# Performance work log

Hardware: AMD Instinct MI355X
Metric: run time of the kernel (lower is better)

The kernel has to match this reference:

```python
import jax, jax.numpy as jnp
import numpy as np


def setup_inputs() -> dict:
    key = jax.random.key(0)
    k1, k2 = jax.random.split(key)
    query_features = jax.random.normal(k1, (8, 2048, 256), dtype=jnp.float32)   # (B, S, D)
    support_weights = jax.random.normal(k2, (20, 256), dtype=jnp.float32)       # (N, D)
    return {"query_features": query_features, "support_weights": support_weights}


def reference(query_features, support_weights):
    # Original: transpose query to (B, D, S), repeat channels n_cls times,
    # grouped conv1d with groups = n_cls*D, group_size=1, kernel_size=1, padding=0.
    # That is exactly a per-(class, channel) scale of the query features.
    B, S, D = query_features.shape
    N = support_weights.shape[0]
    q = jnp.transpose(query_features, (0, 2, 1))            # (B, D, S)
    # out[b, n, c, s] = q[b, c, s] * w[n, c]
    out = q[:, None, :, :] * support_weights[None, :, :, None]  # (B, N, D, S)
    return out.reshape(B * N, D, S)                          # (B*N, D, S)
```

## Files before the change

### kernel.cpp

```cpp
#include <hip/hip_runtime.h>


namespace {
constexpr int kB = 8;
constexpr int kS = 2048;
constexpr int kD = 256;
constexpr int kN = 20;
constexpr int TS = 512;
constexpr int TC = 16;
constexpr int PTS = TS + 4;
}

__global__ __launch_bounds__(256)
void frw_kernel(const float* __restrict__ q, const float* __restrict__ w,
                float* __restrict__ out) {
  const int s0 = blockIdx.x * TS;
  const int c0 = blockIdx.y * TC;
  const int b  = blockIdx.z;
  const int t  = threadIdx.x;

  __shared__ float tile[TC][PTS];
  __shared__ float ws[kN][TC];

  for (int i = t; i < kN * TC; i += 256) {
    const int n  = i / TC;
    const int cc = i % TC;
    ws[n][cc] = w[n * kD + c0 + cc];
  }

  {
    const int lane4 = t & 3;
    const int srow  = t >> 2;
    const int cvec  = lane4 * 4;
#pragma unroll
    for (int k = 0; k < 8; ++k) {
      const int ss = srow + k * 64;
      const float4 v = *reinterpret_cast<const float4*>(
          &q[((size_t)b * kS + (size_t)(s0 + ss)) * kD + (c0 + cvec)]);
      tile[cvec + 0][ss] = v.x;
      tile[cvec + 1][ss] = v.y;
      tile[cvec + 2][ss] = v.z;
      tile[cvec + 3][ss] = v.w;
    }
  }
  __syncthreads();

  const int half = t >> 7;
  const int soff = (t & 127) * 4;
  for (int n = 0; n < kN; ++n) {
    const size_t base_bn = ((size_t)(b * kN + n)) * kD;
#pragma unroll
    for (int rg = 0; rg < TC / 2; ++rg) {
      const int r = rg * 2 + half;
      const float sc = ws[n][r];
      const float4 v = *reinterpret_cast<const float4*>(&tile[r][soff]);
      float4 o;
      o.x = v.x * sc;
      o.y = v.y * sc;
      o.z = v.z * sc;
      o.w = v.w * sc;
      *reinterpret_cast<float4*>(
          &out[(base_bn + (size_t)(c0 + r)) * kS + (size_t)(s0 + soff)]) = o;
    }
  }
}

extern "C" void kernel_launch(void* const* d_in, const int* in_sizes, int n_in,
                              void* d_out, int out_size, void* d_ws, size_t ws_size,
                              hipStream_t stream) {
  const float* q = (const float*)d_in[0];
  const float* w = (const float*)d_in[1];
  float* out = (float*)d_out;

  dim3 grid(kS / TS, kD / TC, kB);
  frw_kernel<<<grid, 256, 0, stream>>>(q, w, out);
}
```

Before: 341.1 us.

## Give each wavefront a full channel row held in registers, with nontemporal stores

The shared-memory transpose tile is replaced by a per-wavefront mapping: each wave owns one channel across the whole sequence. It loads that channel's query values with strided scalar loads into 32 registers and keeps all 20 weights in registers. Output rows are then written as vectorized nontemporal stores so the large write stream does not pollute cache. The change removes LDS traffic and the barrier, but the query reads become uncoalesced strided loads, and the grid shrinks to 512 blocks.

```diff
diff --git a/kernel.cpp b/kernel.cpp
--- a/kernel.cpp
+++ b/kernel.cpp
@@ -6,61 +6,45 @@
 constexpr int kS = 2048;
 constexpr int kD = 256;
 constexpr int kN = 20;
-constexpr int TS = 512;
-constexpr int TC = 16;
-constexpr int PTS = TS + 4;
+
+typedef float v4f __attribute__((ext_vector_type(4)));
 }
 
 __global__ __launch_bounds__(256)
 void frw_kernel(const float* __restrict__ q, const float* __restrict__ w,
                 float* __restrict__ out) {
-  const int s0 = blockIdx.x * TS;
-  const int c0 = blockIdx.y * TC;
-  const int b  = blockIdx.z;
-  const int t  = threadIdx.x;
+  const int lane = threadIdx.x & 63;
+  const int wv   = threadIdx.x >> 6;
+  const int c    = blockIdx.x * 4 + wv;
+  const int b    = blockIdx.y;
 
-  __shared__ float tile[TC][PTS];
-  __shared__ float ws[kN][TC];
+  float wreg[kN];
+#pragma unroll
+  for (int n = 0; n < kN; ++n) wreg[n] = w[n * kD + c];
 
-  for (int i = t; i < kN * TC; i += 256) {
-    const int n  = i / TC;
-    const int cc = i % TC;
-    ws[n][cc] = w[n * kD + c0 + cc];
+  float qv[8][4];
+  const float* qb = q + (size_t)b * kS * kD + c;
+#pragma unroll
+  for (int k = 0; k < 8; ++k) {
+#pragma unroll
+    for (int j = 0; j < 4; ++j) {
+      qv[k][j] = qb[(size_t)(k * 256 + 4 * lane + j) * kD];
+    }
   }
 
-  {
-    const int lane4 = t & 3;
-    const int srow  = t >> 2;
-    const int cvec  = lane4 * 4;
+  float* ob = out + ((size_t)(b * kN) * kD + (size_t)c) * kS + 4 * lane;
+#pragma unroll
+  for (int n = 0; n < kN; ++n) {
+    const float sc = wreg[n];
+    float* orow = ob + (size_t)n * kD * kS;
 #pragma unroll
     for (int k = 0; k < 8; ++k) {
-      const int ss = srow + k * 64;
-      const float4 v = *reinterpret_cast<const float4*>(
-          &q[((size_t)b * kS + (size_t)(s0 + ss)) * kD + (c0 + cvec)]);
-      tile[cvec + 0][ss] = v.x;
-      tile[cvec + 1][ss] = v.y;
-      tile[cvec + 2][ss] = v.z;
-      tile[cvec + 3][ss] = v.w;
-    }
-  }
-  __syncthreads();
-
-  const int half = t >> 7;
-  const int soff = (t & 127) * 4;
-  for (int n = 0; n < kN; ++n) {
-    const size_t base_bn = ((size_t)(b * kN + n)) * kD;
-#pragma unroll
-    for (int rg = 0; rg < TC / 2; ++rg) {
-      const int r = rg * 2 + half;
-      const float sc = ws[n][r];
-      const float4 v = *reinterpret_cast<const float4*>(&tile[r][soff]);
-      float4 o;
-      o.x = v.x * sc;
-      o.y = v.y * sc;
-      o.z = v.z * sc;
-      o.w = v.w * sc;
-      *reinterpret_cast<float4*>(
-          &out[(base_bn + (size_t)(c0 + r)) * kS + (size_t)(s0 + soff)]) = o;
+      v4f o;
+      o.x = qv[k][0] * sc;
+      o.y = qv[k][1] * sc;
+      o.z = qv[k][2] * sc;
+      o.w = qv[k][3] * sc;
+      __builtin_nontemporal_store(o, reinterpret_cast<v4f*>(orow + k * 256));
     }
   }
 }
@@ -72,6 +56,6 @@
   const float* w = (const float*)d_in[1];
   float* out = (float*)d_out;
 
-  dim3 grid(kS / TS, kD / TC, kB);
+  dim3 grid(kD / 4, kB, 1);
   frw_kernel<<<grid, 256, 0, stream>>>(q, w, out);
 }
```

Measured after the change: 355.6 us. +4.3%, slower.
